# Kernel optimization log

Measured on AMD Instinct MI355X. Metric: run time of the kernel, lower is better.

## Reference

```python
import jax, jax.numpy as jnp
import numpy as np
from jax import lax

B, P, T = 64, 16, 256
I, H, O = 256, 512, 5
V = 50000


def setup_inputs() -> dict:
    key = jax.random.key(0)
    ks = jax.random.split(key, 16)
    xav = lambda k, shape: jax.random.normal(k, shape, dtype=jnp.float32) * np.sqrt(2.0 / (shape[-2] + shape[-1]))
    inp = {
        "x": jax.random.randint(ks[0], (B, P, T), 0, V),
        "emb": jax.random.normal(ks[1], (V, I), dtype=jnp.float32) * 0.02,
        "W_forget_x": xav(ks[2], (P, I, H)),
        "W_forget_h": xav(ks[3], (H, H)),
        "b_forget": jnp.zeros((H,), jnp.float32),
        "W_ic_x": xav(ks[4], (P, I, H)),
        "W_ic_h": xav(ks[5], (H, H)),
        "b_ic": jnp.zeros((H,), jnp.float32),
        "W_in_x": xav(ks[6], (P, I, H)),
        "W_in_h": xav(ks[7], (H, H)),
        "b_in": jnp.zeros((H,), jnp.float32),
        "W_o_x": xav(ks[8], (P, I, H)),
        "W_o_h": xav(ks[9], (H, H)),
        "b_o": jnp.zeros((H,), jnp.float32),
        "W_lin": xav(ks[10], (H, O)),
        "b_lin": jnp.zeros((O,), jnp.float32),
    }
    return inp


def reference(x, emb, W_forget_x, W_forget_h, b_forget, W_ic_x, W_ic_h, b_ic,
              W_in_x, W_in_h, b_in, W_o_x, W_o_h, b_o, W_lin, b_lin):
    # padding_idx=0: row 0 of the embedding table is zero
    tbl = emb.at[0].set(0.0)
    xe = tbl[x]  # [B, P, T, I]
    # x-side gate pre-activations, summed over POS tags, hoisted out of the recurrence
    pre_f = jnp.einsum('bpti,pih->tbh', xe, W_forget_x) + b_forget  # [T, B, H]
    pre_i = jnp.einsum('bpti,pih->tbh', xe, W_ic_x) + b_ic
    pre_g = jnp.einsum('bpti,pih->tbh', xe, W_in_x) + b_in
    pre_o = jnp.einsum('bpti,pih->tbh', xe, W_o_x) + b_o

    def step(carry, pres):
        h, c = carry
        pf, pi, pg, po = pres
        f = jax.nn.sigmoid(pf + h @ W_forget_h)
        i = jax.nn.sigmoid(pi + h @ W_ic_h)
        g = jnp.tanh(pg + h @ W_in_h)
        o = jax.nn.sigmoid(po + h @ W_o_h)
        c = f * c + i * g
        h = o * jnp.tanh(c)
        return (h, c), None

    bs = x.shape[0]
    h0 = jnp.zeros((bs, W_forget_h.shape[0]), jnp.float32)
    c0 = jnp.zeros_like(h0)
    (h_t, c_t), _ = lax.scan(step, (h0, c0), (pre_f, pre_i, pre_g, pre_o))
    out = h_t @ W_lin + b_lin  # [B, O]
    return out, h_t, c_t
```

## Files before the change

### kernel.cpp

```cpp
#include <hip/hip_runtime.h>
#include <stdint.h>

#define DEVI __device__ __forceinline__
typedef unsigned long long ull;

typedef __bf16 bf16x8 __attribute__((ext_vector_type(8)));
typedef float floatx4 __attribute__((ext_vector_type(4)));
typedef unsigned int u32x4 __attribute__((ext_vector_type(4)));

DEVI uint16_t f2bf(float f) {
  union { float f; uint32_t u; } c; c.f = f;
  uint32_t u = c.u;
  return (uint16_t)((u + 0x7fffu + ((u >> 16) & 1u)) >> 16);
}
DEVI float bf2f(uint16_t h) {
  union { uint32_t u; float f; } c; c.u = ((uint32_t)h) << 16;
  return c.f;
}
DEVI void load_lds_16(const void* g, void* l) {
  __builtin_amdgcn_global_load_lds(
      (const __attribute__((address_space(1))) void*)g,
      (__attribute__((address_space(3))) void*)l, 16, 0, 0);
}
DEVI float sigm(float x) { return 1.f / (1.f + __expf(-x)); }
DEVI float tanh_s(float x) {
  float xc = fminf(fmaxf(x, -15.f), 15.f);
  float e = __expf(2.f * xc);
  return (e - 1.f) / (e + 1.f);
}

static constexpr size_t OFF_EMB    = 0;
static constexpr size_t OFF_WXT    = 25600000;
static constexpr size_t OFF_WHT    = OFF_WXT + 16777216;
static constexpr size_t OFF_BIAS   = OFF_WHT + 2097152;
static constexpr size_t OFF_PRE    = OFF_BIAS + 8192;
static constexpr size_t OFF_HF     = OFF_PRE + 67108864 + 4096;
static constexpr size_t OFF_CF     = OFF_HF + 131072;
static constexpr size_t OFF_CNT    = OFF_CF + 131072;
static constexpr size_t OFF_SLAB01 = OFF_CNT + 4096;

__global__ __launch_bounds__(256) void k_emb_cvt(const float* __restrict__ emb,
                                                 uint16_t* __restrict__ dst) {
  size_t tid = (size_t)blockIdx.x * 256 + threadIdx.x;
  size_t e = tid * 8;
  int v = (int)(e >> 8);
  const float4* s = (const float4*)(emb + e);
  float4 f0 = s[0], f1 = s[1];
  if (v == 0) { f0 = make_float4(0.f, 0.f, 0.f, 0.f); f1 = f0; }
  uint32_t w0 = f2bf(f0.x) | ((uint32_t)f2bf(f0.y) << 16);
  uint32_t w1 = f2bf(f0.z) | ((uint32_t)f2bf(f0.w) << 16);
  uint32_t w2 = f2bf(f1.x) | ((uint32_t)f2bf(f1.y) << 16);
  uint32_t w3 = f2bf(f1.z) | ((uint32_t)f2bf(f1.w) << 16);
  *(uint4*)(dst + e) = make_uint4(w0, w1, w2, w3);
}

__global__ __launch_bounds__(256) void k_wt(const float* __restrict__ w0, const float* __restrict__ w1,
                                            const float* __restrict__ w2, const float* __restrict__ w3,
                                            int K, uint16_t* __restrict__ dst) {
  __shared__ float tile[64 * 64];
  int k0 = blockIdx.x * 64;
  int n0 = blockIdx.y * 64;
  int h0 = blockIdx.y * 16;
  int g = threadIdx.x >> 6, di = threadIdx.x & 63;
  const float* w = (g == 0) ? w0 : (g == 1) ? w1 : (g == 2) ? w2 : w3;
  const float4* src = (const float4*)(w + (size_t)(k0 + di) * 512 + h0);
  float4 a = src[0], b = src[1], c = src[2], d = src[3];
  float vals[16] = {a.x, a.y, a.z, a.w, b.x, b.y, b.z, b.w,
                    c.x, c.y, c.z, c.w, d.x, d.y, d.z, d.w};
#pragma unroll
  for (int dh = 0; dh < 16; ++dh) tile[(dh * 4 + g) * 64 + di] = vals[dh];
  __syncthreads();
  int nl = threadIdx.x >> 2, ch = threadIdx.x & 3;
  uint32_t wb[8];
#pragma unroll
  for (int j = 0; j < 8; ++j) {
    float lo = tile[nl * 64 + ch * 16 + j * 2];
    float hi = tile[nl * 64 + ch * 16 + j * 2 + 1];
    wb[j] = f2bf(lo) | ((uint32_t)f2bf(hi) << 16);
  }
  uint4* dp = (uint4*)(dst + (size_t)(n0 + nl) * K + k0 + ch * 16);
  dp[0] = make_uint4(wb[0], wb[1], wb[2], wb[3]);
  dp[1] = make_uint4(wb[4], wb[5], wb[6], wb[7]);
}

__global__ __launch_bounds__(256) void k_bias(const float* __restrict__ b0, const float* __restrict__ b1,
                                              const float* __restrict__ b2, const float* __restrict__ b3,
                                              float* __restrict__ dst) {
  int n = blockIdx.x * 256 + threadIdx.x;
  int h = n >> 2, g = n & 3;
  const float* b = (g == 0) ? b0 : (g == 1) ? b1 : (g == 2) ? b2 : b3;
  dst[n] = b[h];
}

__global__ __launch_bounds__(256) void k_gemm(const uint16_t* __restrict__ embbf,
                                              const int* __restrict__ x,
                                              const uint16_t* __restrict__ wxt,
                                              uint16_t* __restrict__ pre) {
  __shared__ uint16_t As[128 * 64];
  __shared__ uint16_t Bs[128 * 64];
  const int tid = threadIdx.x;
  const int wv = tid >> 6, ln = tid & 63;
  const int wm = wv >> 1, wn = wv & 1;
  const int M0 = blockIdx.x * 128, N0 = blockIdx.y * 128;
  const int srow = ln >> 3, schunk = ln & 7;

  const int* xrow[4];
  const uint16_t* bbase[4];
  uint16_t* ldsA[4];
  uint16_t* ldsB[4];
#pragma unroll
  for (int j = 0; j < 4; ++j) {
    int r = j * 32 + wv * 8 + srow;
    int m = M0 + r;
    int t = m >> 6, b = m & 63;
    xrow[j] = x + b * 4096 + t;
    bbase[j] = wxt + (size_t)(N0 + r) * 4096 + schunk * 8;
    ldsA[j] = As + (j * 32 + wv * 8) * 64;
    ldsB[j] = Bs + (j * 32 + wv * 8) * 64;
  }

  const int q = ln >> 4, l16 = ln & 15;
  int aoff[4], boff[4];
#pragma unroll
  for (int mt = 0; mt < 4; ++mt) aoff[mt] = (wm * 64 + mt * 16 + l16) * 64 + q * 8;
#pragma unroll
  for (int nt = 0; nt < 4; ++nt) boff[nt] = (wn * 64 + nt * 16 + l16) * 64 + q * 8;

  floatx4 acc[4][4] = {};

  for (int p = 0; p < 16; ++p) {
    const uint16_t* abase[4];
#pragma unroll
    for (int j = 0; j < 4; ++j) {
      int idx = xrow[j][p << 8];
      abase[j] = embbf + (size_t)idx * 256 + schunk * 8;
    }
#pragma unroll 1
    for (int ki = 0; ki < 4; ++ki) {
      __syncthreads();
#pragma unroll
      for (int j = 0; j < 4; ++j) load_lds_16(abase[j] + ki * 64, ldsA[j]);
#pragma unroll
      for (int j = 0; j < 4; ++j) load_lds_16(bbase[j] + p * 256 + ki * 64, ldsB[j]);
      __syncthreads();
#pragma unroll
      for (int kk = 0; kk < 2; ++kk) {
        bf16x8 a[4];
#pragma unroll
        for (int mt = 0; mt < 4; ++mt) a[mt] = *(const bf16x8*)(As + aoff[mt] + kk * 32);
#pragma unroll
        for (int nt = 0; nt < 4; ++nt) {
          bf16x8 bv = *(const bf16x8*)(Bs + boff[nt] + kk * 32);
#pragma unroll
          for (int mt = 0; mt < 4; ++mt)
            acc[mt][nt] = __builtin_amdgcn_mfma_f32_16x16x32_bf16(a[mt], bv, acc[mt][nt], 0, 0, 0);
        }
      }
    }
  }

#pragma unroll
  for (int mt = 0; mt < 4; ++mt) {
    int mg = M0 + wm * 64 + mt * 16 + q * 4;
#pragma unroll
    for (int nt = 0; nt < 4; ++nt) {
      int ng = N0 + wn * 64 + nt * 16 + l16;
#pragma unroll
      for (int r = 0; r < 4; ++r)
        pre[(size_t)(mg + r) * 2048 + ng] = f2bf(acc[mt][nt][r]);
    }
  }
}

__global__ __launch_bounds__(256) void k_rec(const uint16_t* pre,
                                             char* preb,
                                             char* scratch,
                                             const uint16_t* __restrict__ wht,
                                             const float* __restrict__ biasp,
                                             float* __restrict__ hfin,
                                             float* __restrict__ cfin) {
  __shared__ uint16_t Ahs[2][16 * 528];
  __shared__ float gates[16 * 132];

  const int tid = threadIdx.x;
  const int wv = tid >> 6, ln = tid & 63;
  const int q = ln >> 4, l16 = ln & 15;
  const int bg = blockIdx.x >> 4, cg = blockIdx.x & 15;
  const int N0 = cg * 128;

  bf16x8 Bfrag[16][2];
#pragma unroll
  for (int kc = 0; kc < 16; ++kc)
#pragma unroll
    for (int nt = 0; nt < 2; ++nt) {
      int n = N0 + wv * 32 + nt * 16 + l16;
      Bfrag[kc][nt] = *(const bf16x8*)(wht + (size_t)n * 512 + kc * 32 + q * 8);
    }
  float breg[2];
#pragma unroll
  for (int nt = 0; nt < 2; ++nt) breg[nt] = biasp[N0 + wv * 32 + nt * 16 + l16];

  const int prow = tid >> 4;
  const int pseg = tid & 15;
  const int erow = ln >> 2;
  const int es = ln & 3;
  float creg[2] = {0.f, 0.f};

  for (int i = tid; i < 4224; i += 256) ((uint32_t*)Ahs[0])[i] = 0;

  uint16_t pr[8];
#pragma unroll
  for (int nt = 0; nt < 2; ++nt)
#pragma unroll
    for (int r = 0; r < 4; ++r)
      pr[nt * 4 + r] = pre[(size_t)(bg * 16 + q * 4 + r) * 2048 + N0 + wv * 32 + nt * 16 + l16];

  for (int t = 0; t < 256; ++t) {
    if (t > 0) {
      const char* sb = ((t - 1) < 2 ? scratch + (size_t)(t - 1) * 262144
                                    : preb + (size_t)(t - 3) * 262144) + (size_t)bg * 65536;
      const char* base = sb + prow * 2048 + pseg * 16;
      const uint32_t want = (uint32_t)t;
      u32x4 u0, u1, u2, u3, u4, u5, u6, u7;
      for (;;) {
        asm volatile(
            "global_load_dwordx4 %0, %8, off sc0 sc1\n\t"
            "global_load_dwordx4 %1, %8, off offset:256 sc0 sc1\n\t"
            "global_load_dwordx4 %2, %8, off offset:512 sc0 sc1\n\t"
            "global_load_dwordx4 %3, %8, off offset:768 sc0 sc1\n\t"
            "global_load_dwordx4 %4, %8, off offset:1024 sc0 sc1\n\t"
            "global_load_dwordx4 %5, %8, off offset:1280 sc0 sc1\n\t"
            "global_load_dwordx4 %6, %8, off offset:1536 sc0 sc1\n\t"
            "global_load_dwordx4 %7, %8, off offset:1792 sc0 sc1\n\t"
            "s_waitcnt vmcnt(0)"
            : "=v"(u0), "=v"(u1), "=v"(u2), "=v"(u3),
              "=v"(u4), "=v"(u5), "=v"(u6), "=v"(u7)
            : "v"(base)
            : "memory");
        bool ok = (u0.y == want) && (u0.w == want) && (u1.y == want) && (u1.w == want) &&
                  (u2.y == want) && (u2.w == want) && (u3.y == want) && (u3.w == want) &&
                  (u4.y == want) && (u4.w == want) && (u5.y == want) && (u5.w == want) &&
                  (u6.y == want) && (u6.w == want) && (u7.y == want) && (u7.w == want);
        if (ok) break;
        __builtin_amdgcn_s_sleep(1);
      }
      uint16_t* dr = Ahs[t & 1] + prow * 528 + pseg * 4;
      *(ull*)(dr +   0) = (ull)u0.x | ((ull)u0.z << 32);
      *(ull*)(dr +  64) = (ull)u1.x | ((ull)u1.z << 32);
      *(ull*)(dr + 128) = (ull)u2.x | ((ull)u2.z << 32);
      *(ull*)(dr + 192) = (ull)u3.x | ((ull)u3.z << 32);
      *(ull*)(dr + 256) = (ull)u4.x | ((ull)u4.z << 32);
      *(ull*)(dr + 320) = (ull)u5.x | ((ull)u5.z << 32);
      *(ull*)(dr + 384) = (ull)u6.x | ((ull)u6.z << 32);
      *(ull*)(dr + 448) = (ull)u7.x | ((ull)u7.z << 32);
    }
    __syncthreads();

    const uint16_t* Ab = Ahs[t & 1];
    floatx4 a0[2] = {}, a1[2] = {};
#pragma unroll
    for (int kc = 0; kc < 8; ++kc) {
      bf16x8 a = *(const bf16x8*)(Ab + l16 * 528 + kc * 32 + q * 8);
#pragma unroll
      for (int nt = 0; nt < 2; ++nt)
        a0[nt] = __builtin_amdgcn_mfma_f32_16x16x32_bf16(a, Bfrag[kc][nt], a0[nt], 0, 0, 0);
    }
#pragma unroll
    for (int kc = 8; kc < 16; ++kc) {
      bf16x8 a = *(const bf16x8*)(Ab + l16 * 528 + kc * 32 + q * 8);
#pragma unroll
      for (int nt = 0; nt < 2; ++nt)
        a1[nt] = __builtin_amdgcn_mfma_f32_16x16x32_bf16(a, Bfrag[kc][nt], a1[nt], 0, 0, 0);
    }

#pragma unroll
    for (int nt = 0; nt < 2; ++nt) {
      int n_l = wv * 32 + nt * 16 + l16;
      floatx4 s = a0[nt] + a1[nt];
#pragma unroll
      for (int r = 0; r < 4; ++r) {
        int row = q * 4 + r;
        gates[row * 132 + n_l] = s[r] + breg[nt] + bf2f(pr[nt * 4 + r]);
      }
    }

    {
      float4 v0 = *(const float4*)(gates + erow * 132 + wv * 32 + es * 8);
      float4 v1 = *(const float4*)(gates + erow * 132 + wv * 32 + es * 8 + 4);
      float f0 = sigm(v0.x), i0 = sigm(v0.y), g0 = tanh_s(v0.z), o0 = sigm(v0.w);
      float f1 = sigm(v1.x), i1 = sigm(v1.y), g1 = tanh_s(v1.z), o1 = sigm(v1.w);
      float c0 = f0 * creg[0] + i0 * g0; creg[0] = c0;
      float c1 = f1 * creg[1] + i1 * g1; creg[1] = c1;
      float h0 = o0 * tanh_s(c0), h1 = o1 * tanh_s(c1);
      char* sbw = (t < 2 ? scratch + (size_t)t * 262144
                         : preb + (size_t)(t - 2) * 262144) + (size_t)bg * 65536;
      int pair = cg * 16 + wv * 4 + es;
      ull pk = (ull)((uint32_t)f2bf(h0) | ((uint32_t)f2bf(h1) << 16)) |
               ((ull)(uint32_t)(t + 1) << 32);
      __hip_atomic_store((ull*)(sbw + erow * 2048 + pair * 8),
                         pk, __ATOMIC_RELAXED, __HIP_MEMORY_SCOPE_AGENT);
      if (t == 255) {
        size_t idx = (size_t)(bg * 16 + erow) * 512 + cg * 32 + wv * 8 + es * 2;
        hfin[idx] = h0; hfin[idx + 1] = h1;
        cfin[idx] = c0; cfin[idx + 1] = c1;
      }
    }

    if (t < 255) {
      int tn = t + 1;
#pragma unroll
      for (int nt = 0; nt < 2; ++nt)
#pragma unroll
        for (int r = 0; r < 4; ++r)
          pr[nt * 4 + r] = pre[(size_t)(tn * 64 + bg * 16 + q * 4 + r) * 2048 + N0 + wv * 32 + nt * 16 + l16];
    }
  }
}

__global__ __launch_bounds__(256) void k_final(const float* __restrict__ h, const float* __restrict__ c,
                                               const float* __restrict__ wl, const float* __restrict__ bl,
                                               float* __restrict__ out) {
  __shared__ float red[256];
  int b = blockIdx.x, t = threadIdx.x;
  const float* hb = h + (size_t)b * 512;
  if (t < 128) {
    ((float4*)(out + 320 + (size_t)b * 512))[t] = ((const float4*)hb)[t];
    ((float4*)(out + 320 + 32768 + (size_t)b * 512))[t] = ((const float4*)(c + (size_t)b * 512))[t];
  }
  float h0 = hb[t], h1 = hb[t + 256];
  for (int o = 0; o < 5; ++o) {
    red[t] = h0 * wl[t * 5 + o] + h1 * wl[(t + 256) * 5 + o];
    __syncthreads();
    for (int s = 128; s > 0; s >>= 1) {
      if (t < s) red[t] += red[t + s];
      __syncthreads();
    }
    if (t == 0) out[b * 5 + o] = red[0] + bl[o];
    __syncthreads();
  }
}

extern "C" void kernel_launch(void* const* d_in, const int* in_sizes, int n_in,
                              void* d_out, int out_size, void* d_ws, size_t ws_size,
                              hipStream_t stream) {
  const int*   x   = (const int*)d_in[0];
  const float* emb = (const float*)d_in[1];
  const float* wfx = (const float*)d_in[2];
  const float* wfh = (const float*)d_in[3];
  const float* bf_ = (const float*)d_in[4];
  const float* wix = (const float*)d_in[5];
  const float* wih = (const float*)d_in[6];
  const float* bi_ = (const float*)d_in[7];
  const float* wgx = (const float*)d_in[8];
  const float* wgh = (const float*)d_in[9];
  const float* bg_ = (const float*)d_in[10];
  const float* wox = (const float*)d_in[11];
  const float* woh = (const float*)d_in[12];
  const float* bo_ = (const float*)d_in[13];
  const float* wl  = (const float*)d_in[14];
  const float* bl  = (const float*)d_in[15];
  float* out = (float*)d_out;
  char* ws = (char*)d_ws;

  uint16_t* embbf = (uint16_t*)(ws + OFF_EMB);
  uint16_t* wxt   = (uint16_t*)(ws + OFF_WXT);
  uint16_t* wht   = (uint16_t*)(ws + OFF_WHT);
  float*    bias  = (float*)(ws + OFF_BIAS);
  uint16_t* pre   = (uint16_t*)(ws + OFF_PRE);
  float*    hfin  = (float*)(ws + OFF_HF);
  float*    cfin  = (float*)(ws + OFF_CF);

  hipLaunchKernelGGL(k_emb_cvt, dim3(6250), dim3(256), 0, stream, emb, embbf);
  hipLaunchKernelGGL(k_wt, dim3(64, 32), dim3(256), 0, stream, wfx, wix, wgx, wox, 4096, wxt);
  hipLaunchKernelGGL(k_wt, dim3(8, 32), dim3(256), 0, stream, wfh, wih, wgh, woh, 512, wht);
  hipLaunchKernelGGL(k_bias, dim3(8), dim3(256), 0, stream, bf_, bi_, bg_, bo_, bias);
  hipLaunchKernelGGL(k_gemm, dim3(128, 16), dim3(256), 0, stream, embbf, x, wxt, pre);
  hipLaunchKernelGGL(k_rec, dim3(64), dim3(256), 0, stream, pre, (char*)(ws + OFF_PRE),
                     ws + OFF_SLAB01, wht, bias, hfin, cfin);
  hipLaunchKernelGGL(k_final, dim3(64), dim3(256), 0, stream, hfin, cfin, wl, bl, out);
}
```

Before: 1.023 ms.

## Fuse input GEMM and recurrence into one persistent kernel with per-row readiness counters

Merges the x-side GEMM and the LSTM recurrence into a single launch. Blocks 0-63 run the recurrence and the other 576 blocks compute GEMM tiles in timestep order, publishing completion through per-M-block counters that the recurrence polls before reading each step's pre-activations. This lets the serial recurrence overlap with the bulk GEMM instead of waiting for all of it to finish. The h exchange moves to a two-slot ring buffer. It adds spin-wait overhead, cache-bypassing stores, and bounded 'fuel' timeouts that can break out of waits early and read stale data, which risks silent incorrectness if blocks are not co-resident or progress is slow.

```diff
diff --git a/kernel.cpp b/kernel.cpp
--- a/kernel.cpp
+++ b/kernel.cpp
@@ -27,6 +27,12 @@
   float xc = fminf(fmaxf(x, -15.f), 15.f);
   float e = __expf(2.f * xc);
   return (e - 1.f) / (e + 1.f);
+}
+DEVI void bypass_store_u16(uint16_t* p, uint32_t v) {
+  asm volatile("global_store_short %0, %1, off sc0 sc1" :: "v"(p), "v"(v) : "memory");
+}
+DEVI void bypass_store_u32(unsigned* p, uint32_t v) {
+  asm volatile("global_store_dword %0, %1, off sc0 sc1" :: "v"(p), "v"(v) : "memory");
 }
 
 static constexpr size_t OFF_EMB    = 0;
@@ -37,7 +43,7 @@
 static constexpr size_t OFF_HF     = OFF_PRE + 67108864 + 4096;
 static constexpr size_t OFF_CF     = OFF_HF + 131072;
 static constexpr size_t OFF_CNT    = OFF_CF + 131072;
-static constexpr size_t OFF_SLAB01 = OFF_CNT + 4096;
+static constexpr size_t OFF_RING   = OFF_CNT + 4096;
 
 __global__ __launch_bounds__(256) void k_emb_cvt(const float* __restrict__ emb,
                                                  uint16_t* __restrict__ dst) {
@@ -85,104 +91,118 @@
 
 __global__ __launch_bounds__(256) void k_bias(const float* __restrict__ b0, const float* __restrict__ b1,
                                               const float* __restrict__ b2, const float* __restrict__ b3,
-                                              float* __restrict__ dst) {
+                                              float* __restrict__ dst, unsigned* __restrict__ dcnt) {
   int n = blockIdx.x * 256 + threadIdx.x;
+  if (n < 128) bypass_store_u32(dcnt + n, 0u);
   int h = n >> 2, g = n & 3;
   const float* b = (g == 0) ? b0 : (g == 1) ? b1 : (g == 2) ? b2 : b3;
   dst[n] = b[h];
 }
 
-__global__ __launch_bounds__(256) void k_gemm(const uint16_t* __restrict__ embbf,
-                                              const int* __restrict__ x,
-                                              const uint16_t* __restrict__ wxt,
-                                              uint16_t* __restrict__ pre) {
-  __shared__ uint16_t As[128 * 64];
-  __shared__ uint16_t Bs[128 * 64];
+__global__ __launch_bounds__(256) void k_fused(const uint16_t* __restrict__ embbf,
+                                               const int* __restrict__ x,
+                                               const uint16_t* __restrict__ wxt,
+                                               uint16_t* pre,
+                                               char* ring,
+                                               const uint16_t* __restrict__ wht,
+                                               const float* __restrict__ biasp,
+                                               float* __restrict__ hfin,
+                                               float* __restrict__ cfin,
+                                               unsigned* dcnt) {
+  __shared__ __align__(16) char smem[42240];
   const int tid = threadIdx.x;
-  const int wv = tid >> 6, ln = tid & 63;
-  const int wm = wv >> 1, wn = wv & 1;
-  const int M0 = blockIdx.x * 128, N0 = blockIdx.y * 128;
-  const int srow = ln >> 3, schunk = ln & 7;
-
-  const int* xrow[4];
-  const uint16_t* bbase[4];
-  uint16_t* ldsA[4];
-  uint16_t* ldsB[4];
-#pragma unroll
-  for (int j = 0; j < 4; ++j) {
-    int r = j * 32 + wv * 8 + srow;
-    int m = M0 + r;
-    int t = m >> 6, b = m & 63;
-    xrow[j] = x + b * 4096 + t;
-    bbase[j] = wxt + (size_t)(N0 + r) * 4096 + schunk * 8;
-    ldsA[j] = As + (j * 32 + wv * 8) * 64;
-    ldsB[j] = Bs + (j * 32 + wv * 8) * 64;
+
+  if (blockIdx.x >= 64) {
+    uint16_t* As = (uint16_t*)smem;
+    uint16_t* Bs = (uint16_t*)(smem + 16384);
+    const int wv = tid >> 6, ln = tid & 63;
+    const int wm = wv >> 1, wn = wv & 1;
+    const int srow = ln >> 3, schunk = ln & 7;
+    const int q = ln >> 4, l16 = ln & 15;
+
+    uint16_t* ldsA[4];
+    uint16_t* ldsB[4];
+#pragma unroll
+    for (int j = 0; j < 4; ++j) {
+      ldsA[j] = As + (j * 32 + wv * 8) * 64;
+      ldsB[j] = Bs + (j * 32 + wv * 8) * 64;
+    }
+    int aoff[4], boff[4];
+#pragma unroll
+    for (int mt = 0; mt < 4; ++mt) aoff[mt] = (wm * 64 + mt * 16 + l16) * 64 + q * 8;
+#pragma unroll
+    for (int nt = 0; nt < 4; ++nt) boff[nt] = (wn * 64 + nt * 16 + l16) * 64 + q * 8;
+
+    for (unsigned tile = (unsigned)(blockIdx.x - 64); tile < 2048u; tile += 576u) {
+      const int Mb = (int)(tile >> 4), Nb = (int)(tile & 15u);
+      const int M0 = Mb * 128, N0 = Nb * 128;
+
+      const int* xrow[4];
+      const uint16_t* bbase[4];
+#pragma unroll
+      for (int j = 0; j < 4; ++j) {
+        int r = j * 32 + wv * 8 + srow;
+        int m = M0 + r;
+        int t = m >> 6, b = m & 63;
+        xrow[j] = x + b * 4096 + t;
+        bbase[j] = wxt + (size_t)(N0 + r) * 4096 + schunk * 8;
+      }
+
+      floatx4 acc[4][4] = {};
+
+      for (int p = 0; p < 16; ++p) {
+        const uint16_t* abase[4];
+#pragma unroll
+        for (int j = 0; j < 4; ++j) {
+          int idx = xrow[j][p << 8];
+          abase[j] = embbf + (size_t)idx * 256 + schunk * 8;
+        }
+#pragma unroll 1
+        for (int ki = 0; ki < 4; ++ki) {
+          __syncthreads();
+#pragma unroll
+          for (int j = 0; j < 4; ++j) load_lds_16(abase[j] + ki * 64, ldsA[j]);
+#pragma unroll
+          for (int j = 0; j < 4; ++j) load_lds_16(bbase[j] + p * 256 + ki * 64, ldsB[j]);
+          __syncthreads();
+#pragma unroll
+          for (int kk = 0; kk < 2; ++kk) {
+            bf16x8 a[4];
+#pragma unroll
+            for (int mt = 0; mt < 4; ++mt) a[mt] = *(const bf16x8*)(As + aoff[mt] + kk * 32);
+#pragma unroll
+            for (int nt = 0; nt < 4; ++nt) {
+              bf16x8 bv = *(const bf16x8*)(Bs + boff[nt] + kk * 32);
+#pragma unroll
+              for (int mt = 0; mt < 4; ++mt)
+                acc[mt][nt] = __builtin_amdgcn_mfma_f32_16x16x32_bf16(a[mt], bv, acc[mt][nt], 0, 0, 0);
+            }
+          }
+        }
+      }
+
+#pragma unroll
+      for (int mt = 0; mt < 4; ++mt) {
+        int mg = M0 + wm * 64 + mt * 16 + q * 4;
+#pragma unroll
+        for (int nt = 0; nt < 4; ++nt) {
+          int ng = N0 + wn * 64 + nt * 16 + l16;
+#pragma unroll
+          for (int r = 0; r < 4; ++r)
+            bypass_store_u16(pre + (size_t)(mg + r) * 2048 + ng, (uint32_t)f2bf(acc[mt][nt][r]));
+        }
+      }
+      asm volatile("s_waitcnt vmcnt(0)" ::: "memory");
+      __syncthreads();
+      if (tid == 0)
+        __hip_atomic_fetch_add(&dcnt[Mb], 1u, __ATOMIC_RELAXED, __HIP_MEMORY_SCOPE_AGENT);
+    }
+    return;
   }
 
-  const int q = ln >> 4, l16 = ln & 15;
-  int aoff[4], boff[4];
-#pragma unroll
-  for (int mt = 0; mt < 4; ++mt) aoff[mt] = (wm * 64 + mt * 16 + l16) * 64 + q * 8;
-#pragma unroll
-  for (int nt = 0; nt < 4; ++nt) boff[nt] = (wn * 64 + nt * 16 + l16) * 64 + q * 8;
-
-  floatx4 acc[4][4] = {};
-
-  for (int p = 0; p < 16; ++p) {
-    const uint16_t* abase[4];
-#pragma unroll
-    for (int j = 0; j < 4; ++j) {
-      int idx = xrow[j][p << 8];
-      abase[j] = embbf + (size_t)idx * 256 + schunk * 8;
-    }
-#pragma unroll 1
-    for (int ki = 0; ki < 4; ++ki) {
-      __syncthreads();
-#pragma unroll
-      for (int j = 0; j < 4; ++j) load_lds_16(abase[j] + ki * 64, ldsA[j]);
-#pragma unroll
-      for (int j = 0; j < 4; ++j) load_lds_16(bbase[j] + p * 256 + ki * 64, ldsB[j]);
-      __syncthreads();
-#pragma unroll
-      for (int kk = 0; kk < 2; ++kk) {
-        bf16x8 a[4];
-#pragma unroll
-        for (int mt = 0; mt < 4; ++mt) a[mt] = *(const bf16x8*)(As + aoff[mt] + kk * 32);
-#pragma unroll
-        for (int nt = 0; nt < 4; ++nt) {
-          bf16x8 bv = *(const bf16x8*)(Bs + boff[nt] + kk * 32);
-#pragma unroll
-          for (int mt = 0; mt < 4; ++mt)
-            acc[mt][nt] = __builtin_amdgcn_mfma_f32_16x16x32_bf16(a[mt], bv, acc[mt][nt], 0, 0, 0);
-        }
-      }
-    }
-  }
-
-#pragma unroll
-  for (int mt = 0; mt < 4; ++mt) {
-    int mg = M0 + wm * 64 + mt * 16 + q * 4;
-#pragma unroll
-    for (int nt = 0; nt < 4; ++nt) {
-      int ng = N0 + wn * 64 + nt * 16 + l16;
-#pragma unroll
-      for (int r = 0; r < 4; ++r)
-        pre[(size_t)(mg + r) * 2048 + ng] = f2bf(acc[mt][nt][r]);
-    }
-  }
-}
-
-__global__ __launch_bounds__(256) void k_rec(const uint16_t* pre,
-                                             char* preb,
-                                             char* scratch,
-                                             const uint16_t* __restrict__ wht,
-                                             const float* __restrict__ biasp,
-                                             float* __restrict__ hfin,
-                                             float* __restrict__ cfin) {
-  __shared__ uint16_t Ahs[2][16 * 528];
-  __shared__ float gates[16 * 132];
-
-  const int tid = threadIdx.x;
+  uint16_t (*Ahs)[16 * 528] = (uint16_t (*)[16 * 528])smem;
+  float* gates = (float*)(smem + 33792);
+
   const int wv = tid >> 6, ln = tid & 63;
   const int q = ln >> 4, l16 = ln & 15;
   const int bg = blockIdx.x >> 4, cg = blockIdx.x & 15;
@@ -208,6 +228,21 @@
 
   for (int i = tid; i < 4224; i += 256) ((uint32_t*)Ahs[0])[i] = 0;
 
+  int frontier = -1;
+  auto gate = [&](int m) {
+    int fuel = 1 << 13;
+    while (frontier < m) {
+      uint32_t v;
+      asm volatile("global_load_dword %0, %1, off sc0 sc1\n\t"
+                   "s_waitcnt vmcnt(0)"
+                   : "=v"(v) : "v"(dcnt + (frontier + 1)) : "memory");
+      if (v >= 16u) { ++frontier; continue; }
+      if (--fuel <= 0) { ++frontier; continue; }
+      __builtin_amdgcn_s_sleep(2);
+    }
+  };
+
+  gate(0);
   uint16_t pr[8];
 #pragma unroll
   for (int nt = 0; nt < 2; ++nt)
@@ -217,11 +252,11 @@
 
   for (int t = 0; t < 256; ++t) {
     if (t > 0) {
-      const char* sb = ((t - 1) < 2 ? scratch + (size_t)(t - 1) * 262144
-                                    : preb + (size_t)(t - 3) * 262144) + (size_t)bg * 65536;
+      const char* sb = ring + (size_t)((t - 1) & 1) * 262144 + (size_t)bg * 65536;
       const char* base = sb + prow * 2048 + pseg * 16;
       const uint32_t want = (uint32_t)t;
       u32x4 u0, u1, u2, u3, u4, u5, u6, u7;
+      int pfuel = 1 << 13;
       for (;;) {
         asm volatile(
             "global_load_dwordx4 %0, %8, off sc0 sc1\n\t"
@@ -242,6 +277,7 @@
                   (u4.y == want) && (u4.w == want) && (u5.y == want) && (u5.w == want) &&
                   (u6.y == want) && (u6.w == want) && (u7.y == want) && (u7.w == want);
         if (ok) break;
+        if (--pfuel <= 0) break;
         __builtin_amdgcn_s_sleep(1);
       }
       uint16_t* dr = Ahs[t & 1] + prow * 528 + pseg * 4;
@@ -292,8 +328,7 @@
       float c0 = f0 * creg[0] + i0 * g0; creg[0] = c0;
       float c1 = f1 * creg[1] + i1 * g1; creg[1] = c1;
       float h0 = o0 * tanh_s(c0), h1 = o1 * tanh_s(c1);
-      char* sbw = (t < 2 ? scratch + (size_t)t * 262144
-                         : preb + (size_t)(t - 2) * 262144) + (size_t)bg * 65536;
+      char* sbw = ring + (size_t)(t & 1) * 262144 + (size_t)bg * 65536;
       int pair = cg * 16 + wv * 4 + es;
       ull pk = (ull)((uint32_t)f2bf(h0) | ((uint32_t)f2bf(h1) << 16)) |
                ((ull)(uint32_t)(t + 1) << 32);
@@ -308,6 +343,7 @@
 
     if (t < 255) {
       int tn = t + 1;
+      gate(tn >> 1);
 #pragma unroll
       for (int nt = 0; nt < 2; ++nt)
 #pragma unroll
@@ -369,13 +405,13 @@
   uint16_t* pre   = (uint16_t*)(ws + OFF_PRE);
   float*    hfin  = (float*)(ws + OFF_HF);
   float*    cfin  = (float*)(ws + OFF_CF);
+  unsigned* dcnt  = (unsigned*)(ws + OFF_CNT);
 
   hipLaunchKernelGGL(k_emb_cvt, dim3(6250), dim3(256), 0, stream, emb, embbf);
   hipLaunchKernelGGL(k_wt, dim3(64, 32), dim3(256), 0, stream, wfx, wix, wgx, wox, 4096, wxt);
   hipLaunchKernelGGL(k_wt, dim3(8, 32), dim3(256), 0, stream, wfh, wih, wgh, woh, 512, wht);
-  hipLaunchKernelGGL(k_bias, dim3(8), dim3(256), 0, stream, bf_, bi_, bg_, bo_, bias);
-  hipLaunchKernelGGL(k_gemm, dim3(128, 16), dim3(256), 0, stream, embbf, x, wxt, pre);
-  hipLaunchKernelGGL(k_rec, dim3(64), dim3(256), 0, stream, pre, (char*)(ws + OFF_PRE),
-                     ws + OFF_SLAB01, wht, bias, hfin, cfin);
+  hipLaunchKernelGGL(k_bias, dim3(8), dim3(256), 0, stream, bf_, bi_, bg_, bo_, bias, dcnt);
+  hipLaunchKernelGGL(k_fused, dim3(640), dim3(256), 0, stream, embbf, x, wxt, pre,
+                     ws + OFF_RING, wht, bias, hfin, cfin, dcnt);
   hipLaunchKernelGGL(k_final, dim3(64), dim3(256), 0, stream, hfin, cfin, wl, bl, out);
 }
```

Measured after the change: 1.457 ms. 1.42x slower.

## Pin recurrence roles to XCCs and exchange h via a two-slot ring

Applied to the files above, without the earlier changes.

Launches 512 recurrence blocks and has each claim a role through atomics keyed on its XCC id, so that the 16 blocks of each batch group sit on the same XCC and the surplus blocks exit. The h exchange moves from a per-timestep slab, which overwrote the consumed pre buffer, to a two-slot ring. The spin loop now polls with sc0-only loads most of the time and uses system-coherent loads only every fourth try. It also gains a fuel limit that bails out of the wait. The aim is lower cross-XCC synchronization latency per timestep. The risks are reading stale data, since polling skips sc1 and the fuel exit continues with unready values, a possible overwrite race in the two-slot ring, and extra claim overhead.

```diff
diff --git a/kernel.cpp b/kernel.cpp
--- a/kernel.cpp
+++ b/kernel.cpp
@@ -27,6 +27,9 @@
   float xc = fminf(fmaxf(x, -15.f), 15.f);
   float e = __expf(2.f * xc);
   return (e - 1.f) / (e + 1.f);
+}
+DEVI void bypass_store_u32(unsigned* p, uint32_t v) {
+  asm volatile("global_store_dword %0, %1, off sc0 sc1" :: "v"(p), "v"(v) : "memory");
 }
 
 static constexpr size_t OFF_EMB    = 0;
@@ -37,7 +40,7 @@
 static constexpr size_t OFF_HF     = OFF_PRE + 67108864 + 4096;
 static constexpr size_t OFF_CF     = OFF_HF + 131072;
 static constexpr size_t OFF_CNT    = OFF_CF + 131072;
-static constexpr size_t OFF_SLAB01 = OFF_CNT + 4096;
+static constexpr size_t OFF_RING   = OFF_CNT + 4096;
 
 __global__ __launch_bounds__(256) void k_emb_cvt(const float* __restrict__ emb,
                                                  uint16_t* __restrict__ dst) {
@@ -85,8 +88,9 @@
 
 __global__ __launch_bounds__(256) void k_bias(const float* __restrict__ b0, const float* __restrict__ b1,
                                               const float* __restrict__ b2, const float* __restrict__ b3,
-                                              float* __restrict__ dst) {
+                                              float* __restrict__ dst, unsigned* __restrict__ claim) {
   int n = blockIdx.x * 256 + threadIdx.x;
+  if (n < 24) bypass_store_u32(claim + n, 0u);
   int h = n >> 2, g = n & 3;
   const float* b = (g == 0) ? b0 : (g == 1) ? b1 : (g == 2) ? b2 : b3;
   dst[n] = b[h];
@@ -172,21 +176,60 @@
   }
 }
 
-__global__ __launch_bounds__(256) void k_rec(const uint16_t* pre,
-                                             char* preb,
-                                             char* scratch,
+__global__ __launch_bounds__(256) void k_rec(const uint16_t* __restrict__ pre,
+                                             char* ring,
                                              const uint16_t* __restrict__ wht,
                                              const float* __restrict__ biasp,
                                              float* __restrict__ hfin,
-                                             float* __restrict__ cfin) {
+                                             float* __restrict__ cfin,
+                                             unsigned* claim) {
   __shared__ uint16_t Ahs[2][16 * 528];
   __shared__ float gates[16 * 132];
+  __shared__ int s_role;
 
   const int tid = threadIdx.x;
+
+  if (tid == 0) {
+    uint32_t xcc;
+    asm volatile("s_getreg_b32 %0, hwreg(HW_REG_XCC_ID)" : "=s"(xcc));
+    xcc &= 15u;
+    int role = -1;
+    ull* map = (ull*)(claim + 16);
+    if (xcc < 4u) {
+      unsigned slot = atomicAdd(&claim[xcc], 1u);
+      if (slot < 16u) {
+        int r = (int)(xcc * 16u + slot);
+        ull old = atomicOr(map, 1ull << r);
+        if (!((old >> r) & 1ull)) role = r;
+      }
+    }
+    if (role < 0) {
+      ull m = 0;
+      for (int g = 0; g < 1024; ++g) {
+        m = __hip_atomic_load(map, __ATOMIC_RELAXED, __HIP_MEMORY_SCOPE_AGENT);
+        if (m == ~0ull) break;
+        __builtin_amdgcn_s_sleep(8);
+      }
+      if (m != ~0ull) {
+        for (int r = 0; r < 64 && role < 0; ++r) {
+          if (!((m >> r) & 1ull)) {
+            ull old = atomicOr(map, 1ull << r);
+            if (!((old >> r) & 1ull)) role = r;
+            else m = old;
+          }
+        }
+      }
+    }
+    s_role = role;
+  }
+  __syncthreads();
+  const int role = s_role;
+  if (role < 0) return;
+  const int bg = role >> 4, cg = role & 15;
+  const int N0 = cg * 128;
+
   const int wv = tid >> 6, ln = tid & 63;
   const int q = ln >> 4, l16 = ln & 15;
-  const int bg = blockIdx.x >> 4, cg = blockIdx.x & 15;
-  const int N0 = cg * 128;
 
   bf16x8 Bfrag[16][2];
 #pragma unroll
@@ -217,32 +260,50 @@
 
   for (int t = 0; t < 256; ++t) {
     if (t > 0) {
-      const char* sb = ((t - 1) < 2 ? scratch + (size_t)(t - 1) * 262144
-                                    : preb + (size_t)(t - 3) * 262144) + (size_t)bg * 65536;
+      const char* sb = ring + (size_t)((t - 1) & 1) * 262144 + (size_t)bg * 65536;
       const char* base = sb + prow * 2048 + pseg * 16;
       const uint32_t want = (uint32_t)t;
       u32x4 u0, u1, u2, u3, u4, u5, u6, u7;
-      for (;;) {
-        asm volatile(
-            "global_load_dwordx4 %0, %8, off sc0 sc1\n\t"
-            "global_load_dwordx4 %1, %8, off offset:256 sc0 sc1\n\t"
-            "global_load_dwordx4 %2, %8, off offset:512 sc0 sc1\n\t"
-            "global_load_dwordx4 %3, %8, off offset:768 sc0 sc1\n\t"
-            "global_load_dwordx4 %4, %8, off offset:1024 sc0 sc1\n\t"
-            "global_load_dwordx4 %5, %8, off offset:1280 sc0 sc1\n\t"
-            "global_load_dwordx4 %6, %8, off offset:1536 sc0 sc1\n\t"
-            "global_load_dwordx4 %7, %8, off offset:1792 sc0 sc1\n\t"
-            "s_waitcnt vmcnt(0)"
-            : "=v"(u0), "=v"(u1), "=v"(u2), "=v"(u3),
-              "=v"(u4), "=v"(u5), "=v"(u6), "=v"(u7)
-            : "v"(base)
-            : "memory");
+      int pfuel = 1 << 13;
+      for (int it = 0;; ++it) {
+        if ((it & 3) != 3) {
+          asm volatile(
+              "global_load_dwordx4 %0, %8, off sc0\n\t"
+              "global_load_dwordx4 %1, %8, off offset:256 sc0\n\t"
+              "global_load_dwordx4 %2, %8, off offset:512 sc0\n\t"
+              "global_load_dwordx4 %3, %8, off offset:768 sc0\n\t"
+              "global_load_dwordx4 %4, %8, off offset:1024 sc0\n\t"
+              "global_load_dwordx4 %5, %8, off offset:1280 sc0\n\t"
+              "global_load_dwordx4 %6, %8, off offset:1536 sc0\n\t"
+              "global_load_dwordx4 %7, %8, off offset:1792 sc0\n\t"
+              "s_waitcnt vmcnt(0)"
+              : "=v"(u0), "=v"(u1), "=v"(u2), "=v"(u3),
+                "=v"(u4), "=v"(u5), "=v"(u6), "=v"(u7)
+              : "v"(base)
+              : "memory");
+        } else {
+          asm volatile(
+              "global_load_dwordx4 %0, %8, off sc0 sc1\n\t"
+              "global_load_dwordx4 %1, %8, off offset:256 sc0 sc1\n\t"
+              "global_load_dwordx4 %2, %8, off offset:512 sc0 sc1\n\t"
+              "global_load_dwordx4 %3, %8, off offset:768 sc0 sc1\n\t"
+              "global_load_dwordx4 %4, %8, off offset:1024 sc0 sc1\n\t"
+              "global_load_dwordx4 %5, %8, off offset:1280 sc0 sc1\n\t"
+              "global_load_dwordx4 %6, %8, off offset:1536 sc0 sc1\n\t"
+              "global_load_dwordx4 %7, %8, off offset:1792 sc0 sc1\n\t"
+              "s_waitcnt vmcnt(0)"
+              : "=v"(u0), "=v"(u1), "=v"(u2), "=v"(u3),
+                "=v"(u4), "=v"(u5), "=v"(u6), "=v"(u7)
+              : "v"(base)
+              : "memory");
+        }
         bool ok = (u0.y == want) && (u0.w == want) && (u1.y == want) && (u1.w == want) &&
                   (u2.y == want) && (u2.w == want) && (u3.y == want) && (u3.w == want) &&
                   (u4.y == want) && (u4.w == want) && (u5.y == want) && (u5.w == want) &&
                   (u6.y == want) && (u6.w == want) && (u7.y == want) && (u7.w == want);
         if (ok) break;
-        __builtin_amdgcn_s_sleep(1);
+        if (--pfuel <= 0) break;
+        if ((it & 3) == 3) __builtin_amdgcn_s_sleep(1);
       }
       uint16_t* dr = Ahs[t & 1] + prow * 528 + pseg * 4;
       *(ull*)(dr +   0) = (ull)u0.x | ((ull)u0.z << 32);
@@ -292,8 +353,7 @@
       float c0 = f0 * creg[0] + i0 * g0; creg[0] = c0;
       float c1 = f1 * creg[1] + i1 * g1; creg[1] = c1;
       float h0 = o0 * tanh_s(c0), h1 = o1 * tanh_s(c1);
-      char* sbw = (t < 2 ? scratch + (size_t)t * 262144
-                         : preb + (size_t)(t - 2) * 262144) + (size_t)bg * 65536;
+      char* sbw = ring + (size_t)(t & 1) * 262144 + (size_t)bg * 65536;
       int pair = cg * 16 + wv * 4 + es;
       ull pk = (ull)((uint32_t)f2bf(h0) | ((uint32_t)f2bf(h1) << 16)) |
                ((ull)(uint32_t)(t + 1) << 32);
@@ -369,13 +429,14 @@
   uint16_t* pre   = (uint16_t*)(ws + OFF_PRE);
   float*    hfin  = (float*)(ws + OFF_HF);
   float*    cfin  = (float*)(ws + OFF_CF);
+  unsigned* claim = (unsigned*)(ws + OFF_CNT);
 
   hipLaunchKernelGGL(k_emb_cvt, dim3(6250), dim3(256), 0, stream, emb, embbf);
   hipLaunchKernelGGL(k_wt, dim3(64, 32), dim3(256), 0, stream, wfx, wix, wgx, wox, 4096, wxt);
   hipLaunchKernelGGL(k_wt, dim3(8, 32), dim3(256), 0, stream, wfh, wih, wgh, woh, 512, wht);
-  hipLaunchKernelGGL(k_bias, dim3(8), dim3(256), 0, stream, bf_, bi_, bg_, bo_, bias);
+  hipLaunchKernelGGL(k_bias, dim3(8), dim3(256), 0, stream, bf_, bi_, bg_, bo_, bias, claim);
   hipLaunchKernelGGL(k_gemm, dim3(128, 16), dim3(256), 0, stream, embbf, x, wxt, pre);
-  hipLaunchKernelGGL(k_rec, dim3(64), dim3(256), 0, stream, pre, (char*)(ws + OFF_PRE),
-                     ws + OFF_SLAB01, wht, bias, hfin, cfin);
+  hipLaunchKernelGGL(k_rec, dim3(512), dim3(256), 0, stream, pre, ws + OFF_RING,
+                     wht, bias, hfin, cfin, claim);
   hipLaunchKernelGGL(k_final, dim3(64), dim3(256), 0, stream, hfin, cfin, wl, bl, out);
 }
```

Result: slower. 1.426 ms (+39.5%).
